# Kernel tuning notes

Measured on AMD Instinct MI355X. Metric: run time of the kernel, lower is better.

The kernel has to match this reference:

```python
import jax, jax.numpy as jnp
import numpy as np

N = 20000      # nodes
L = 64         # seq_length
E = 64         # emb_size
V = 30000      # vocab_size
HG = 128       # gnn_hidden_size
HT = 128       # text_hidden_size
NE = 640000    # edges
EPS = 1e-12


def _normalize(x):
    # F.normalize(x, p=2, dim=1) on [N, E, L]
    n = jnp.sqrt(jnp.sum(x * x, axis=1, keepdims=True))
    return x / jnp.maximum(n, EPS)


def gcn_conv(x, W, b, src_idx, dst_idx, n_nodes):
    # PyG GCNConv: add self-loops, symmetric normalization D^-1/2 (A+I) D^-1/2 (X W) + b
    h = x @ W                                            # [N, out]
    deg = jnp.zeros((n_nodes,), h.dtype).at[dst_idx].add(1.0) + 1.0  # incl. self-loop
    dinv = jax.lax.rsqrt(deg)
    norm = dinv[src_idx] * dinv[dst_idx]                 # [NE]
    msg = h[src_idx] * norm[:, None]                     # gather + scale
    out = jnp.zeros_like(h).at[dst_idx].add(msg)         # scatter-add to targets
    out = out + h * (dinv * dinv)[:, None]               # self-loop term
    return out + b


def setup_inputs() -> dict:
    key = jax.random.key(0)
    ks = jax.random.split(key, 12)
    rn = lambda k, shape: jax.random.normal(k, shape, jnp.float32) * 0.02
    return {
        "src": jax.random.randint(ks[0], (N, L), 0, V),
        "seg": jax.random.randint(ks[1], (N, L), 0, 3),
        "edge_index": jax.random.randint(ks[2], (2, NE), 0, N),
        "src_emb": rn(ks[3], (V, E)),
        "seg_emb": rn(ks[4], (3, E)),
        "w": jnp.ones((L,), jnp.float32),
        "Wq1": rn(ks[5], (E, HT)), "bq1": jnp.zeros((HT,), jnp.float32),
        "Wq2": rn(ks[6], (HT, E)), "bq2": jnp.zeros((E,), jnp.float32),
        "Wg1": rn(ks[7], (E, HG)), "bg1": jnp.zeros((HG,), jnp.float32),
        "Wg2": rn(ks[8], (HG, E)), "bg2": jnp.zeros((E,), jnp.float32),
        "Wl": rn(ks[9], (E, E)),   "bl": jnp.zeros((E,), jnp.float32),
    }


def reference(src, seg, edge_index, src_emb, seg_emb, w, Wq1, bq1, Wq2, bq2,
              Wg1, bg1, Wg2, bg2, Wl, bl):
    # --- LiteratureEmbedding ---
    se = src_emb[src]                 # [N, L, E]
    ge = seg_emb[seg]                 # [N, L, E]
    sv = se.reshape(-1, E, L)         # raw view (matches torch .view, not transpose)
    gv = ge.reshape(-1, E, L)
    f = (_normalize(w * sv) + _normalize(gv)).sum(-1)   # [N, E]
    # --- query MLP ---
    x = jax.nn.relu(f @ Wq1 + bq1) @ Wq2 + bq2
    # --- two GCN layers ---
    si, di = edge_index[0], edge_index[1]
    x = jax.nn.relu(gcn_conv(x, Wg1, bg1, si, di, N))
    x = jax.nn.relu(gcn_conv(x, Wg2, bg2, si, di, N))
    # --- output linear (dropout is identity in eval) ---
    return x @ Wl + bl
```

## Files before the change

kernel.cpp:

```cpp
#include <hip/hip_runtime.h>

#if defined(__has_builtin)
#if __has_builtin(__builtin_amdgcn_readlane)
#define READLANE(v, l) __builtin_amdgcn_readlane((v), (l))
#else
#define READLANE(v, l) __shfl((v), (l))
#endif
#else
#define READLANE(v, l) __shfl((v), (l))
#endif
__device__ __forceinline__ float readlane_f(float v, int l) {
    return __uint_as_float(READLANE(__float_as_uint(v), l));
}

__device__ __forceinline__ unsigned short f2bf(float x) {
    unsigned u = __float_as_uint(x);
    u += 0x7FFFu + ((u >> 16) & 1u);
    return (unsigned short)(u >> 16);
}
__device__ __forceinline__ float bfl(unsigned u) { return __uint_as_float(u << 16); }
__device__ __forceinline__ float bfh(unsigned u) { return __uint_as_float(u & 0xFFFF0000u); }

#define CAPLOG 8
#define EPB 10

__global__ __launch_bounds__(256) void hist_k(
    const int* __restrict__ di, int ne, int* __restrict__ bhist)
{
    __shared__ int lh[512];
    const int t = threadIdx.x;
    for (int i = t; i < 512; i += 256) lh[i] = 0;
    __syncthreads();
    const int base = blockIdx.x * (256 * EPB);
    #pragma unroll
    for (int r = 0; r < EPB; ++r) {
        int i = base + r * 256 + t;
        if (i < ne) atomicAdd(&lh[di[i] >> 6], 1);
    }
    __syncthreads();
    for (int i = t; i < 512; i += 256)
        if (lh[i]) atomicAdd(&bhist[i], lh[i]);
}

__global__ __launch_bounds__(256) void scan_k(
    const int* __restrict__ bhist, int* __restrict__ boff,
    int* __restrict__ bcur, int nb,
    unsigned* __restrict__ Cz, unsigned* __restrict__ Az)
{
    __shared__ int sh[512];
    const int t = threadIdx.x;
    for (int i = t; i < 512; i += 256) sh[i] = (i < nb) ? bhist[i] : 0;
    __syncthreads();
    if (t == 0) {
        int run = 0;
        for (int i = 0; i < nb; ++i) { int v = sh[i]; sh[i] = run; run += v; }
    }
    __syncthreads();
    for (int i = t; i < 512; i += 256)
        if (i < nb) { boff[i] = sh[i]; bcur[i] = sh[i]; }
    if (t < 32) { Cz[t] = 0u; Az[t] = 0u; }
}

__global__ __launch_bounds__(256) void prep0b_k(
    const int* __restrict__ si, const int* __restrict__ di, int ne,
    int* __restrict__ bcur, unsigned* __restrict__ pairs, int pB,
    const float* __restrict__ src_emb, unsigned short* __restrict__ sbf, int ve)
{
    const int t = threadIdx.x;
    if ((int)blockIdx.x < pB) {
        __shared__ int lh[512];
        __shared__ int lbase[512];
        for (int i = t; i < 512; i += 256) lh[i] = 0;
        __syncthreads();
        int bb[EPB], rk[EPB];
        unsigned pk[EPB];
        const int base = blockIdx.x * (256 * EPB);
        #pragma unroll
        for (int r = 0; r < EPB; ++r) {
            int i = base + r * 256 + t;
            if (i < ne) {
                int d = di[i], s = si[i];
                int b = d >> 6;
                bb[r] = b;
                rk[r] = atomicAdd(&lh[b], 1);
                pk[r] = ((unsigned)(d & 63) << 20) | (unsigned)s;
            } else bb[r] = -1;
        }
        __syncthreads();
        for (int i = t; i < 512; i += 256)
            if (lh[i]) lbase[i] = atomicAdd(&bcur[i], lh[i]);
        __syncthreads();
        #pragma unroll
        for (int r = 0; r < EPB; ++r)
            if (bb[r] >= 0) pairs[lbase[bb[r]] + rk[r]] = pk[r];
        return;
    }
    int i = (((int)blockIdx.x - pB) * 256 + t) * 4;
    if (i + 3 < ve) {
        float4 v = *(const float4*)&src_emb[i];
        ushort4 u;
        u.x = f2bf(v.x); u.y = f2bf(v.y); u.z = f2bf(v.z); u.w = f2bf(v.w);
        *(ushort4*)&sbf[i] = u;
    } else {
        for (; i < ve; ++i) sbf[i] = f2bf(src_emb[i]);
    }
}

__global__ __launch_bounds__(256) void binfill_k(
    const unsigned* __restrict__ pairs, const int* __restrict__ bhist,
    const int* __restrict__ boff, int* __restrict__ edge_off,
    int* __restrict__ deg, int nN)
{
    __shared__ int cntL[64];
    __shared__ int slotsL[64 * 256];
    const int t = threadIdx.x;
    const int b = blockIdx.x;
    if (t < 64) cntL[t] = 0;
    __syncthreads();
    const int ne_b = bhist[b];
    const int st   = boff[b];
    for (int k = t; k < ne_b; k += 256) {
        unsigned pk = pairs[st + k];
        int dl = (int)(pk >> 20);
        int s  = (int)(pk & 0xFFFFFu);
        int p  = atomicAdd(&cntL[dl], 1);
        if (p < 256) slotsL[dl * 256 + p] = s << 7;
    }
    __syncthreads();
    if (t < 64) {
        int node = (b << 6) + t;
        if (node < nN) deg[node] = cntL[t];
    }
    const int wv = t >> 6, j = t & 63;
    const int dl = wv * 16 + (j >> 2);
    const int k0 = j & 3;
    const int node = (b << 6) + dl;
    if (node < nN) {
        const int c = min(cntL[dl], 256);
        for (int k = k0; k < c; k += 4)
            edge_off[((long)node << CAPLOG) + k] = slotsL[dl * 256 + k];
    }
}

__global__ __launch_bounds__(256) void prep1_k(
    const int* __restrict__ src, const int* __restrict__ seg,
    const unsigned short* __restrict__ sbf, const float* __restrict__ seg_emb,
    const float* __restrict__ wvec, float* __restrict__ f, int nN)
{
    __shared__ float scr[4][16 * 66];
    const int t = threadIdx.x;
    const int wid = t >> 6, q = t & 63;
    const long n = (long)blockIdx.x * 4 + wid;
    if (n >= nN) return;
    const int grp = q >> 4, c = q & 15;

    const int off = src[n * 64 + q] << 7;
    const int sg  = seg[n * 64 + q];
    const float e0 = seg_emb[q], e1 = seg_emb[64 + q], e2 = seg_emb[128 + q];
    const char* base = (const char*)sbf;

    uint2 dreg[16];
    #pragma unroll
    for (int i = 0; i < 16; ++i) {
        int ro = __shfl(off, i * 4 + grp);
        dreg[i] = *(const uint2*)(base + (ro + c * 8));
    }

    float t0 = 0.f, t1 = 0.f, t2 = 0.f, t3 = 0.f;
    #pragma unroll
    for (int i = 0; i < 16; ++i) {
        float v0 = bfl(dreg[i].x);
        float v1 = bfh(dreg[i].x);
        float v2 = bfl(dreg[i].y);
        float v3 = bfh(dreg[i].y);
        t0 += v0 * v0; t1 += v1 * v1; t2 += v2 * v2; t3 += v3 * v3;
    }
    t0 += __shfl_xor(t0, 16); t0 += __shfl_xor(t0, 32);
    t1 += __shfl_xor(t1, 16); t1 += __shfl_xor(t1, 32);
    t2 += __shfl_xor(t2, 16); t2 += __shfl_xor(t2, 32);
    t3 += __shfl_xor(t3, 16); t3 += __shfl_xor(t3, 32);

    const float4 wv = *(const float4*)&wvec[c * 4];
    float4 cf;
    cf.x = wv.x / fmaxf(fabsf(wv.x) * sqrtf(t0), 1e-12f);
    cf.y = wv.y / fmaxf(fabsf(wv.y) * sqrtf(t1), 1e-12f);
    cf.z = wv.z / fmaxf(fabsf(wv.z) * sqrtf(t2), 1e-12f);
    cf.w = wv.w / fmaxf(fabsf(wv.w) * sqrtf(t3), 1e-12f);

    unsigned long long b0 = __ballot(sg == 0);
    unsigned long long b1 = __ballot(sg == 1);
    float n0 = (float)__popcll(b0), n1 = (float)__popcll(b1);
    float n2 = 64.f - n0 - n1;
    float g2 = n0 * e0 * e0 + n1 * e1 * e1 + n2 * e2 * e2;
    float rg = 1.f / fmaxf(sqrtf(g2), 1e-12f);
    float p0 = e0 * rg, p1 = e1 * rg, p2 = e2 * rg;
    #pragma unroll
    for (int m = 1; m < 64; m <<= 1) {
        p0 += __shfl_xor(p0, m);
        p1 += __shfl_xor(p1, m);
        p2 += __shfl_xor(p2, m);
    }

    float* sw = scr[wid];
    #pragma unroll
    for (int i = 0; i < 16; ++i) {
        float po = bfl(dreg[i].x) * cf.x + bfh(dreg[i].x) * cf.y
                 + bfl(dreg[i].y) * cf.z + bfh(dreg[i].y) * cf.w;
        sw[c * 66 + i * 4 + grp] = po;
    }
    float out = 0.f;
    #pragma unroll
    for (int c2 = 0; c2 < 16; ++c2)
        out += sw[c2 * 66 + q];

    const float dg = (sg == 0) ? p0 : ((sg == 1) ? p1 : p2);
    f[n * 64 + q] = out + dg;
}

#define ACC8(d, a, b)                                                    \
    { (a).x += bfl((d).x); (a).y += bfh((d).x);                          \
      (a).z += bfl((d).y); (a).w += bfh((d).y);                          \
      (b).x += bfl((d).z); (b).y += bfh((d).z);                          \
      (b).z += bfl((d).w); (b).w += bfh((d).w); }

__device__ __forceinline__ void csr_gather16(const char* __restrict__ hb,
                                             const int* __restrict__ eo,
                                             int dn, int j, int zoff,
                                             float4& s0, float4& s1)
{
    const int grp = j >> 3;
    const int col = (j & 7) << 4;
    float4 a0 = make_float4(0.f, 0.f, 0.f, 0.f), a1 = a0;
    float4 b0 = a0, b1 = a0;
    for (int e = 0; e < dn; e += 64) {
        const int cnt = min(dn - e, 64);
        const int eoff = (e + j < dn) ? eo[e + j] : zoff;
        int m = 0;
        for (; m + 16 <= cnt; m += 16) {
            int o0 = __shfl(eoff, m + grp);
            int o1 = __shfl(eoff, m + 8 + grp);
            uint4 d0 = *(const uint4*)(hb + (o0 + col));
            uint4 d1 = *(const uint4*)(hb + (o1 + col));
            ACC8(d0, a0, a1); ACC8(d1, b0, b1);
        }
        for (; m < cnt; m += 8) {
            int o = __shfl(eoff, m + grp);
            uint4 d = *(const uint4*)(hb + (o + col));
            ACC8(d, a0, a1);
        }
    }
    a0.x += b0.x; a0.y += b0.y; a0.z += b0.z; a0.w += b0.w;
    a1.x += b1.x; a1.y += b1.y; a1.z += b1.z; a1.w += b1.w;
    #pragma unroll
    for (int m = 8; m < 64; m <<= 1) {
        a0.x += __shfl_xor(a0.x, m); a0.y += __shfl_xor(a0.y, m);
        a0.z += __shfl_xor(a0.z, m); a0.w += __shfl_xor(a0.w, m);
        a1.x += __shfl_xor(a1.x, m); a1.y += __shfl_xor(a1.y, m);
        a1.z += __shfl_xor(a1.z, m); a1.w += __shfl_xor(a1.w, m);
    }
    s0 = a0; s1 = a1;
}

__device__ __forceinline__ void bf_row16(const char* hb, long rowoff, int col,
                                         float4& v0, float4& v1) {
    uint4 d = *(const uint4*)(hb + rowoff + col);
    v0.x = bfl(d.x); v0.y = bfh(d.x); v0.z = bfl(d.y); v0.w = bfh(d.y);
    v1.x = bfl(d.z); v1.y = bfh(d.z); v1.z = bfl(d.w); v1.w = bfh(d.w);
}

template <bool S2_BIAS>
__device__ __forceinline__ void dense_pair_body(
    float* Wh, float* F, float* H,
    const float* __restrict__ W1, const float* __restrict__ b1,
    const float* __restrict__ W2, const float* __restrict__ b2,
    const int* __restrict__ deg, unsigned short* __restrict__ out,
    int row0, int nrows, int t)
{
    for (int i = t * 4; i < 32 * 128; i += 1024)
        *(float4*)&Wh[i] = *(const float4*)&W1[i];
    __syncthreads();

    const int jg = t & 31, rslot = t >> 5;
    const int j0 = jg * 4;
    float4 acc0, acc1;
    {
        float4 b4 = *(const float4*)&b1[j0];
        acc0 = b4; acc1 = b4;
    }
    #pragma unroll 2
    for (int k = 0; k < 32; k += 4) {
        float4 w0 = *(float4*)&Wh[(k + 0) * 128 + j0];
        float4 w1 = *(float4*)&Wh[(k + 1) * 128 + j0];
        float4 w2 = *(float4*)&Wh[(k + 2) * 128 + j0];
        float4 w3 = *(float4*)&Wh[(k + 3) * 128 + j0];
        float4 fa = *(float4*)&F[rslot * 64 + k];
        float4 fb = *(float4*)&F[(rslot + 8) * 64 + k];
        acc0.x += fa.x * w0.x + fa.y * w1.x + fa.z * w2.x + fa.w * w3.x;
        acc0.y += fa.x * w0.y + fa.y * w1.y + fa.z * w2.y + fa.w * w3.y;
        acc0.z += fa.x * w0.z + fa.y * w1.z + fa.z * w2.z + fa.w * w3.z;
        acc0.w += fa.x * w0.w + fa.y * w1.w + fa.z * w2.w + fa.w * w3.w;
        acc1.x += fb.x * w0.x + fb.y * w1.x + fb.z * w2.x + fb.w * w3.x;
        acc1.y += fb.x * w0.y + fb.y * w1.y + fb.z * w2.y + fb.w * w3.y;
        acc1.z += fb.x * w0.z + fb.y * w1.z + fb.z * w2.z + fb.w * w3.z;
        acc1.w += fb.x * w0.w + fb.y * w1.w + fb.z * w2.w + fb.w * w3.w;
    }
    __syncthreads();
    for (int i = t * 4; i < 32 * 128; i += 1024)
        *(float4*)&Wh[i] = *(const float4*)&W1[32 * 128 + i];
    __syncthreads();
    #pragma unroll 2
    for (int k = 0; k < 32; k += 4) {
        float4 w0 = *(float4*)&Wh[(k + 0) * 128 + j0];
        float4 w1 = *(float4*)&Wh[(k + 1) * 128 + j0];
        float4 w2 = *(float4*)&Wh[(k + 2) * 128 + j0];
        float4 w3 = *(float4*)&Wh[(k + 3) * 128 + j0];
        float4 fa = *(float4*)&F[rslot * 64 + 32 + k];
        float4 fb = *(float4*)&F[(rslot + 8) * 64 + 32 + k];
        acc0.x += fa.x * w0.x + fa.y * w1.x + fa.z * w2.x + fa.w * w3.x;
        acc0.y += fa.x * w0.y + fa.y * w1.y + fa.z * w2.y + fa.w * w3.y;
        acc0.z += fa.x * w0.z + fa.y * w1.z + fa.z * w2.z + fa.w * w3.z;
        acc0.w += fa.x * w0.w + fa.y * w1.w + fa.z * w2.w + fa.w * w3.w;
        acc1.x += fb.x * w0.x + fb.y * w1.x + fb.z * w2.x + fb.w * w3.x;
        acc1.y += fb.x * w0.y + fb.y * w1.y + fb.z * w2.y + fb.w * w3.y;
        acc1.z += fb.x * w0.z + fb.y * w1.z + fb.z * w2.z + fb.w * w3.z;
        acc1.w += fb.x * w0.w + fb.y * w1.w + fb.z * w2.w + fb.w * w3.w;
    }
    {
        float4 v;
        v.x = fmaxf(acc0.x, 0.f); v.y = fmaxf(acc0.y, 0.f);
        v.z = fmaxf(acc0.z, 0.f); v.w = fmaxf(acc0.w, 0.f);
        *(float4*)&H[rslot * 128 + j0] = v;
        v.x = fmaxf(acc1.x, 0.f); v.y = fmaxf(acc1.y, 0.f);
        v.z = fmaxf(acc1.z, 0.f); v.w = fmaxf(acc1.w, 0.f);
        *(float4*)&H[(rslot + 8) * 128 + j0] = v;
    }
    __syncthreads();

    for (int i = t * 4; i < 64 * 64; i += 1024)
        *(float4*)&Wh[i] = *(const float4*)&W2[i];
    __syncthreads();
    const int jg2 = t & 15, r2 = t >> 4;
    const int j02 = jg2 * 4;
    float4 acc = S2_BIAS ? *(const float4*)&b2[j02]
                         : make_float4(0.f, 0.f, 0.f, 0.f);
    #pragma unroll 2
    for (int k = 0; k < 64; k += 4) {
        float4 w0 = *(float4*)&Wh[(k + 0) * 64 + j02];
        float4 w1 = *(float4*)&Wh[(k + 1) * 64 + j02];
        float4 w2 = *(float4*)&Wh[(k + 2) * 64 + j02];
        float4 w3 = *(float4*)&Wh[(k + 3) * 64 + j02];
        float4 fq = *(float4*)&H[r2 * 128 + k];
        acc.x += fq.x * w0.x + fq.y * w1.x + fq.z * w2.x + fq.w * w3.x;
        acc.y += fq.x * w0.y + fq.y * w1.y + fq.z * w2.y + fq.w * w3.y;
        acc.z += fq.x * w0.z + fq.y * w1.z + fq.z * w2.z + fq.w * w3.z;
        acc.w += fq.x * w0.w + fq.y * w1.w + fq.z * w2.w + fq.w * w3.w;
    }
    __syncthreads();
    for (int i = t * 4; i < 64 * 64; i += 1024)
        *(float4*)&Wh[i] = *(const float4*)&W2[64 * 64 + i];
    __syncthreads();
    #pragma unroll 2
    for (int k = 0; k < 64; k += 4) {
        float4 w0 = *(float4*)&Wh[(k + 0) * 64 + j02];
        float4 w1 = *(float4*)&Wh[(k + 1) * 64 + j02];
        float4 w2 = *(float4*)&Wh[(k + 2) * 64 + j02];
        float4 w3 = *(float4*)&Wh[(k + 3) * 64 + j02];
        float4 fq = *(float4*)&H[r2 * 128 + 64 + k];
        acc.x += fq.x * w0.x + fq.y * w1.x + fq.z * w2.x + fq.w * w3.x;
        acc.y += fq.x * w0.y + fq.y * w1.y + fq.z * w2.y + fq.w * w3.y;
        acc.z += fq.x * w0.z + fq.y * w1.z + fq.z * w2.z + fq.w * w3.z;
        acc.w += fq.x * w0.w + fq.y * w1.w + fq.z * w2.w + fq.w * w3.w;
    }
    const int r = row0 + r2;
    if (r < nrows) {
        float sc = rsqrtf((float)deg[r] + 1.0f);
        ushort4 v;
        v.x = f2bf(acc.x * sc); v.y = f2bf(acc.y * sc);
        v.z = f2bf(acc.z * sc); v.w = f2bf(acc.w * sc);
        *(ushort4*)&out[(long)r * 64 + j02] = v;
    }
}

template <bool S2_BIAS>
__global__ __launch_bounds__(256, 5) void fused2_k(
    const float* __restrict__ in, const float* __restrict__ W1,
    const float* __restrict__ b1, const float* __restrict__ W2,
    const float* __restrict__ b2, const int* __restrict__ deg,
    unsigned short* __restrict__ out, int nrows)
{
    __shared__ __align__(16) float Wh[32 * 128];
    __shared__ __align__(16) float F[16 * 64];
    __shared__ __align__(16) float H[16 * 128];
    const int t = threadIdx.x;
    const int row0 = blockIdx.x * 16;

    for (int i = t * 4; i < 16 * 64; i += 1024) {
        int r = i >> 6;
        float4 v = make_float4(0.f, 0.f, 0.f, 0.f);
        if (row0 + r < nrows) v = *(const float4*)&in[(long)row0 * 64 + i];
        *(float4*)&F[i] = v;
    }
    dense_pair_body<S2_BIAS>(Wh, F, H, W1, b1, W2, b2, deg, out, row0, nrows, t);
}

__global__ __launch_bounds__(256, 5) void gcnfused_k(
    const unsigned short* __restrict__ C, const int* __restrict__ deg,
    const int* __restrict__ edge_off,
    const float* __restrict__ W1, const float* __restrict__ b1,
    const float* __restrict__ W2, unsigned short* __restrict__ out,
    int nrows, int zoff)
{
    __shared__ __align__(16) float Wh[32 * 128];
    __shared__ __align__(16) float F[16 * 64];
    __shared__ __align__(16) float H[16 * 128];
    const int t = threadIdx.x;
    const int row0 = blockIdx.x * 16;
    const int wv = t >> 6, j = t & 63;
    const int col = (j & 7) << 4;

    const char* hb = (const char*)C;
    #pragma unroll
    for (int i = 0; i < 4; ++i) {
        const int r = wv * 4 + i;
        const int node = row0 + r;
        if (node < nrows) {
            float4 s0, s1, v0, v1;
            csr_gather16(hb, edge_off + ((long)node << CAPLOG),
                         deg[node], j, zoff, s0, s1);
            bf_row16(hb, (long)node << 7, col, v0, v1);
            float dv = rsqrtf((float)deg[node] + 1.0f);
            if ((j >> 3) == 0) {
                float4 ra, rb;
                ra.x = dv * (v0.x + s0.x); ra.y = dv * (v0.y + s0.y);
                ra.z = dv * (v0.z + s0.z); ra.w = dv * (v0.w + s0.w);
                rb.x = dv * (v1.x + s1.x); rb.y = dv * (v1.y + s1.y);
                rb.z = dv * (v1.z + s1.z); rb.w = dv * (v1.w + s1.w);
                *(float4*)&F[r * 64 + j * 8]     = ra;
                *(float4*)&F[r * 64 + j * 8 + 4] = rb;
            }
        } else if ((j >> 3) == 0) {
            *(float4*)&F[r * 64 + j * 8]     = make_float4(0.f, 0.f, 0.f, 0.f);
            *(float4*)&F[r * 64 + j * 8 + 4] = make_float4(0.f, 0.f, 0.f, 0.f);
        }
    }
    dense_pair_body<false>(Wh, F, H, W1, b1, W2, nullptr, deg, out, row0, nrows, t);
}

__global__ __launch_bounds__(256) void gatherout_k(
    const unsigned short* __restrict__ hp, const int* __restrict__ deg,
    const int* __restrict__ edge_off,
    const float* __restrict__ bg2, const float* __restrict__ Wl,
    const float* __restrict__ bl, float* __restrict__ out, int n, int zoff)
{
    __shared__ __align__(16) float WlL[64 * 64];
    __shared__ __align__(16) float vS[4][64];
    const int t = threadIdx.x;
    for (int i = t * 4; i < 64 * 64; i += 1024)
        *(float4*)&WlL[i] = *(const float4*)&Wl[i];
    __syncthreads();

    const int row0 = blockIdx.x * 16;
    const int wv = t >> 6, j = t & 63;
    const int col = (j & 7) << 4;
    const char* hb = (const char*)hp;
    const float blj = bl[j];
    const float4 bgA = *(const float4*)&bg2[(j & 7) * 8];
    const float4 bgB = *(const float4*)&bg2[(j & 7) * 8 + 4];

    #pragma unroll
    for (int i = 0; i < 4; ++i) {
        const int node = row0 + wv * 4 + i;
        if (node >= n) continue;
        float4 s0, s1, v0, v1;
        csr_gather16(hb, edge_off + ((long)node << CAPLOG),
                     deg[node], j, zoff, s0, s1);
        bf_row16(hb, (long)node << 7, col, v0, v1);
        const float dv = rsqrtf((float)deg[node] + 1.0f);
        float4 fa, fb;
        fa.x = fmaxf(dv * (v0.x + s0.x) + bgA.x, 0.f);
        fa.y = fmaxf(dv * (v0.y + s0.y) + bgA.y, 0.f);
        fa.z = fmaxf(dv * (v0.z + s0.z) + bgA.z, 0.f);
        fa.w = fmaxf(dv * (v0.w + s0.w) + bgA.w, 0.f);
        fb.x = fmaxf(dv * (v1.x + s1.x) + bgB.x, 0.f);
        fb.y = fmaxf(dv * (v1.y + s1.y) + bgB.y, 0.f);
        fb.z = fmaxf(dv * (v1.z + s1.z) + bgB.z, 0.f);
        fb.w = fmaxf(dv * (v1.w + s1.w) + bgB.w, 0.f);
        if ((j >> 3) == 0) {
            *(float4*)&vS[wv][j * 8]     = fa;
            *(float4*)&vS[wv][j * 8 + 4] = fb;
        }
        const float v = vS[wv][j];

        float o = blj;
        #pragma unroll 4
        for (int k = 0; k < 64; k += 4) {
            float vk0 = readlane_f(v, k + 0);
            float vk1 = readlane_f(v, k + 1);
            float vk2 = readlane_f(v, k + 2);
            float vk3 = readlane_f(v, k + 3);
            o += vk0 * WlL[(k + 0) * 64 + j] + vk1 * WlL[(k + 1) * 64 + j]
               + vk2 * WlL[(k + 2) * 64 + j] + vk3 * WlL[(k + 3) * 64 + j];
        }
        out[(long)node * 64 + j] = o;
    }
}

extern "C" void kernel_launch(void* const* d_in, const int* in_sizes, int n_in,
                              void* d_out, int out_size, void* d_ws, size_t ws_size,
                              hipStream_t stream) {
    const int*   src     = (const int*)  d_in[0];
    const int*   seg     = (const int*)  d_in[1];
    const int*   ei      = (const int*)  d_in[2];
    const float* src_emb = (const float*)d_in[3];
    const float* seg_emb = (const float*)d_in[4];
    const float* w       = (const float*)d_in[5];
    const float* Wq1     = (const float*)d_in[6];
    const float* bq1     = (const float*)d_in[7];
    const float* Wq2     = (const float*)d_in[8];
    const float* bq2     = (const float*)d_in[9];
    const float* Wg1     = (const float*)d_in[10];
    const float* bg1     = (const float*)d_in[11];
    const float* Wg2     = (const float*)d_in[12];
    const float* bg2     = (const float*)d_in[13];
    const float* Wl      = (const float*)d_in[14];
    const float* bl      = (const float*)d_in[15];
    float* out = (float*)d_out;

    const int N  = in_sizes[0] / 64;
    const int NE = in_sizes[2] / 2;
    const int VE = in_sizes[3];
    const int* si = ei;
    const int* di = ei + NE;
    const int NB = (N + 63) >> 6;

    const size_t NEpad = ((size_t)NE + 3) & ~(size_t)3;
    const size_t VEpad = ((size_t)VE + 7) & ~(size_t)7;
    int* bhist = (int*)d_ws;
    int* boff  = bhist + 512;
    int* bcur  = boff + 512;
    int* deg   = bcur + 512;
    int* edge_off = deg + (((size_t)N + 3) & ~(size_t)3);
    unsigned* pairs = (unsigned*)(edge_off + ((size_t)N << CAPLOG));
    unsigned short* sbf = (unsigned short*)(pairs + NEpad);
    float* A32 = (float*)(sbf + VEpad);
    unsigned short* Cbf = (unsigned short*)(A32 + (size_t)N * 64);
    unsigned short* Abf = Cbf + (size_t)N * 64 + 64;
    const int zoff = N << 7;

    dim3 b256(256);
    const int convB = (VE + 1023) / 1024;
    const int eBig  = (NE + 256 * EPB - 1) / (256 * EPB);
    const int nB    = (N + 3) / 4;
    const int fB    = (N + 15) / 16;

    hipMemsetAsync(bhist, 0, 512 * sizeof(int), stream);

    hist_k<<<eBig, b256, 0, stream>>>(di, NE, bhist);
    scan_k<<<1, b256, 0, stream>>>(bhist, boff, bcur, NB,
                                   (unsigned*)(Cbf + (size_t)N * 64),
                                   (unsigned*)(Abf + (size_t)N * 64));
    prep0b_k<<<eBig + convB, b256, 0, stream>>>(si, di, NE, bcur, pairs, eBig,
                                                src_emb, sbf, VE);
    binfill_k<<<NB, b256, 0, stream>>>(pairs, bhist, boff, edge_off, deg, N);

    prep1_k<<<nB, b256, 0, stream>>>(src, seg, sbf, seg_emb, w, A32, N);

    fused2_k<true><<<fB, b256, 0, stream>>>(A32, Wq1, bq1, Wq2, bq2,
                                            deg, Cbf, N);

    gcnfused_k<<<fB, b256, 0, stream>>>(Cbf, deg, edge_off,
                                        Wg1, bg1, Wg2, Abf, N, zoff);

    gatherout_k<<<fB, b256, 0, stream>>>(Abf, deg, edge_off, bg2,
                                         Wl, bl, out, N, zoff);
}
```

Before: 215.5 us.

## Merge preprocessing kernels and compute degree via global atomics in histogram pass

The bf16 conversion of the embedding table moves into the histogram kernel, and the per-node embedding/normalization work (formerly prep1_k) now runs as extra blocks of the edge-scatter kernel. This cuts one launch and lets independent work share a grid to fill the GPU. Node degree is now counted with global atomics on deg in the histogram pass instead of being written by binfill, so the memset grows to clear deg. The price is 640k extra global atomics and heavier shared-memory use in the merged scatter kernel.

```diff
diff --git a/kernel.cpp b/kernel.cpp
--- a/kernel.cpp
+++ b/kernel.cpp
@@ -24,22 +24,40 @@
 #define CAPLOG 8
 #define EPB 10
 
-__global__ __launch_bounds__(256) void hist_k(
-    const int* __restrict__ di, int ne, int* __restrict__ bhist)
-{
-    __shared__ int lh[512];
-    const int t = threadIdx.x;
-    for (int i = t; i < 512; i += 256) lh[i] = 0;
-    __syncthreads();
-    const int base = blockIdx.x * (256 * EPB);
-    #pragma unroll
-    for (int r = 0; r < EPB; ++r) {
-        int i = base + r * 256 + t;
-        if (i < ne) atomicAdd(&lh[di[i] >> 6], 1);
-    }
-    __syncthreads();
-    for (int i = t; i < 512; i += 256)
-        if (lh[i]) atomicAdd(&bhist[i], lh[i]);
+__global__ __launch_bounds__(256) void histconv_k(
+    const int* __restrict__ di, int ne, int* __restrict__ bhist,
+    int* __restrict__ deg, int eB,
+    const float* __restrict__ src_emb, unsigned short* __restrict__ sbf, int ve)
+{
+    const int t = threadIdx.x;
+    if ((int)blockIdx.x < eB) {
+        __shared__ int lh[512];
+        for (int i = t; i < 512; i += 256) lh[i] = 0;
+        __syncthreads();
+        const int base = blockIdx.x * (256 * EPB);
+        #pragma unroll
+        for (int r = 0; r < EPB; ++r) {
+            int i = base + r * 256 + t;
+            if (i < ne) {
+                int d = di[i];
+                atomicAdd(&lh[d >> 6], 1);
+                atomicAdd(&deg[d], 1);
+            }
+        }
+        __syncthreads();
+        for (int i = t; i < 512; i += 256)
+            if (lh[i]) atomicAdd(&bhist[i], lh[i]);
+        return;
+    }
+    int i = (((int)blockIdx.x - eB) * 256 + t) * 4;
+    if (i + 3 < ve) {
+        float4 v = *(const float4*)&src_emb[i];
+        ushort4 u;
+        u.x = f2bf(v.x); u.y = f2bf(v.y); u.z = f2bf(v.z); u.w = f2bf(v.w);
+        *(ushort4*)&sbf[i] = u;
+    } else {
+        for (; i < ve; ++i) sbf[i] = f2bf(src_emb[i]);
+    }
 }
 
 __global__ __launch_bounds__(256) void scan_k(
@@ -61,15 +79,18 @@
     if (t < 32) { Cz[t] = 0u; Az[t] = 0u; }
 }
 
-__global__ __launch_bounds__(256) void prep0b_k(
+__global__ __launch_bounds__(256) void scatemb_k(
     const int* __restrict__ si, const int* __restrict__ di, int ne,
     int* __restrict__ bcur, unsigned* __restrict__ pairs, int pB,
-    const float* __restrict__ src_emb, unsigned short* __restrict__ sbf, int ve)
-{
+    const int* __restrict__ src, const int* __restrict__ seg,
+    const unsigned short* __restrict__ sbf, const float* __restrict__ seg_emb,
+    const float* __restrict__ wvec, float* __restrict__ f, int nN)
+{
+    __shared__ __align__(16) float smem[4 * 16 * 66];
     const int t = threadIdx.x;
     if ((int)blockIdx.x < pB) {
-        __shared__ int lh[512];
-        __shared__ int lbase[512];
+        int* lh    = (int*)smem;
+        int* lbase = (int*)smem + 512;
         for (int i = t; i < 512; i += 256) lh[i] = 0;
         __syncthreads();
         int bb[EPB], rk[EPB];
@@ -95,21 +116,77 @@
             if (bb[r] >= 0) pairs[lbase[bb[r]] + rk[r]] = pk[r];
         return;
     }
-    int i = (((int)blockIdx.x - pB) * 256 + t) * 4;
-    if (i + 3 < ve) {
-        float4 v = *(const float4*)&src_emb[i];
-        ushort4 u;
-        u.x = f2bf(v.x); u.y = f2bf(v.y); u.z = f2bf(v.z); u.w = f2bf(v.w);
-        *(ushort4*)&sbf[i] = u;
-    } else {
-        for (; i < ve; ++i) sbf[i] = f2bf(src_emb[i]);
-    }
+    const int wid = t >> 6, q = t & 63;
+    const long n = ((long)blockIdx.x - pB) * 4 + wid;
+    if (n >= nN) return;
+    const int grp = q >> 4, c = q & 15;
+
+    const int off = src[n * 64 + q] << 7;
+    const int sg  = seg[n * 64 + q];
+    const float e0 = seg_emb[q], e1 = seg_emb[64 + q], e2 = seg_emb[128 + q];
+    const char* base = (const char*)sbf;
+
+    uint2 dreg[16];
+    #pragma unroll
+    for (int i = 0; i < 16; ++i) {
+        int ro = __shfl(off, i * 4 + grp);
+        dreg[i] = *(const uint2*)(base + (ro + c * 8));
+    }
+
+    float t0 = 0.f, t1 = 0.f, t2 = 0.f, t3 = 0.f;
+    #pragma unroll
+    for (int i = 0; i < 16; ++i) {
+        float v0 = bfl(dreg[i].x);
+        float v1 = bfh(dreg[i].x);
+        float v2 = bfl(dreg[i].y);
+        float v3 = bfh(dreg[i].y);
+        t0 += v0 * v0; t1 += v1 * v1; t2 += v2 * v2; t3 += v3 * v3;
+    }
+    t0 += __shfl_xor(t0, 16); t0 += __shfl_xor(t0, 32);
+    t1 += __shfl_xor(t1, 16); t1 += __shfl_xor(t1, 32);
+    t2 += __shfl_xor(t2, 16); t2 += __shfl_xor(t2, 32);
+    t3 += __shfl_xor(t3, 16); t3 += __shfl_xor(t3, 32);
+
+    const float4 wv = *(const float4*)&wvec[c * 4];
+    float4 cf;
+    cf.x = wv.x / fmaxf(fabsf(wv.x) * sqrtf(t0), 1e-12f);
+    cf.y = wv.y / fmaxf(fabsf(wv.y) * sqrtf(t1), 1e-12f);
+    cf.z = wv.z / fmaxf(fabsf(wv.z) * sqrtf(t2), 1e-12f);
+    cf.w = wv.w / fmaxf(fabsf(wv.w) * sqrtf(t3), 1e-12f);
+
+    unsigned long long b0 = __ballot(sg == 0);
+    unsigned long long b1 = __ballot(sg == 1);
+    float n0 = (float)__popcll(b0), n1 = (float)__popcll(b1);
+    float n2 = 64.f - n0 - n1;
+    float g2 = n0 * e0 * e0 + n1 * e1 * e1 + n2 * e2 * e2;
+    float rg = 1.f / fmaxf(sqrtf(g2), 1e-12f);
+    float p0 = e0 * rg, p1 = e1 * rg, p2 = e2 * rg;
+    #pragma unroll
+    for (int m = 1; m < 64; m <<= 1) {
+        p0 += __shfl_xor(p0, m);
+        p1 += __shfl_xor(p1, m);
+        p2 += __shfl_xor(p2, m);
+    }
+
+    float* sw = smem + wid * (16 * 66);
+    #pragma unroll
+    for (int i = 0; i < 16; ++i) {
+        float po = bfl(dreg[i].x) * cf.x + bfh(dreg[i].x) * cf.y
+                 + bfl(dreg[i].y) * cf.z + bfh(dreg[i].y) * cf.w;
+        sw[c * 66 + i * 4 + grp] = po;
+    }
+    float out = 0.f;
+    #pragma unroll
+    for (int c2 = 0; c2 < 16; ++c2)
+        out += sw[c2 * 66 + q];
+
+    const float dg = (sg == 0) ? p0 : ((sg == 1) ? p1 : p2);
+    f[n * 64 + q] = out + dg;
 }
 
 __global__ __launch_bounds__(256) void binfill_k(
     const unsigned* __restrict__ pairs, const int* __restrict__ bhist,
-    const int* __restrict__ boff, int* __restrict__ edge_off,
-    int* __restrict__ deg, int nN)
+    const int* __restrict__ boff, int* __restrict__ edge_off, int nN)
 {
     __shared__ int cntL[64];
     __shared__ int slotsL[64 * 256];
@@ -127,10 +204,6 @@
         if (p < 256) slotsL[dl * 256 + p] = s << 7;
     }
     __syncthreads();
-    if (t < 64) {
-        int node = (b << 6) + t;
-        if (node < nN) deg[node] = cntL[t];
-    }
     const int wv = t >> 6, j = t & 63;
     const int dl = wv * 16 + (j >> 2);
     const int k0 = j & 3;
@@ -140,81 +213,6 @@
         for (int k = k0; k < c; k += 4)
             edge_off[((long)node << CAPLOG) + k] = slotsL[dl * 256 + k];
     }
-}
-
-__global__ __launch_bounds__(256) void prep1_k(
-    const int* __restrict__ src, const int* __restrict__ seg,
-    const unsigned short* __restrict__ sbf, const float* __restrict__ seg_emb,
-    const float* __restrict__ wvec, float* __restrict__ f, int nN)
-{
-    __shared__ float scr[4][16 * 66];
-    const int t = threadIdx.x;
-    const int wid = t >> 6, q = t & 63;
-    const long n = (long)blockIdx.x * 4 + wid;
-    if (n >= nN) return;
-    const int grp = q >> 4, c = q & 15;
-
-    const int off = src[n * 64 + q] << 7;
-    const int sg  = seg[n * 64 + q];
-    const float e0 = seg_emb[q], e1 = seg_emb[64 + q], e2 = seg_emb[128 + q];
-    const char* base = (const char*)sbf;
-
-    uint2 dreg[16];
-    #pragma unroll
-    for (int i = 0; i < 16; ++i) {
-        int ro = __shfl(off, i * 4 + grp);
-        dreg[i] = *(const uint2*)(base + (ro + c * 8));
-    }
-
-    float t0 = 0.f, t1 = 0.f, t2 = 0.f, t3 = 0.f;
-    #pragma unroll
-    for (int i = 0; i < 16; ++i) {
-        float v0 = bfl(dreg[i].x);
-        float v1 = bfh(dreg[i].x);
-        float v2 = bfl(dreg[i].y);
-        float v3 = bfh(dreg[i].y);
-        t0 += v0 * v0; t1 += v1 * v1; t2 += v2 * v2; t3 += v3 * v3;
-    }
-    t0 += __shfl_xor(t0, 16); t0 += __shfl_xor(t0, 32);
-    t1 += __shfl_xor(t1, 16); t1 += __shfl_xor(t1, 32);
-    t2 += __shfl_xor(t2, 16); t2 += __shfl_xor(t2, 32);
-    t3 += __shfl_xor(t3, 16); t3 += __shfl_xor(t3, 32);
-
-    const float4 wv = *(const float4*)&wvec[c * 4];
-    float4 cf;
-    cf.x = wv.x / fmaxf(fabsf(wv.x) * sqrtf(t0), 1e-12f);
-    cf.y = wv.y / fmaxf(fabsf(wv.y) * sqrtf(t1), 1e-12f);
-    cf.z = wv.z / fmaxf(fabsf(wv.z) * sqrtf(t2), 1e-12f);
-    cf.w = wv.w / fmaxf(fabsf(wv.w) * sqrtf(t3), 1e-12f);
-
-    unsigned long long b0 = __ballot(sg == 0);
-    unsigned long long b1 = __ballot(sg == 1);
-    float n0 = (float)__popcll(b0), n1 = (float)__popcll(b1);
-    float n2 = 64.f - n0 - n1;
-    float g2 = n0 * e0 * e0 + n1 * e1 * e1 + n2 * e2 * e2;
-    float rg = 1.f / fmaxf(sqrtf(g2), 1e-12f);
-    float p0 = e0 * rg, p1 = e1 * rg, p2 = e2 * rg;
-    #pragma unroll
-    for (int m = 1; m < 64; m <<= 1) {
-        p0 += __shfl_xor(p0, m);
-        p1 += __shfl_xor(p1, m);
-        p2 += __shfl_xor(p2, m);
-    }
-
-    float* sw = scr[wid];
-    #pragma unroll
-    for (int i = 0; i < 16; ++i) {
-        float po = bfl(dreg[i].x) * cf.x + bfh(dreg[i].x) * cf.y
-                 + bfl(dreg[i].y) * cf.z + bfh(dreg[i].y) * cf.w;
-        sw[c * 66 + i * 4 + grp] = po;
-    }
-    float out = 0.f;
-    #pragma unroll
-    for (int c2 = 0; c2 < 16; ++c2)
-        out += sw[c2 * 66 + q];
-
-    const float dg = (sg == 0) ? p0 : ((sg == 1) ? p1 : p2);
-    f[n * 64 + q] = out + dg;
 }
 
 #define ACC8(d, a, b)                                                    \
@@ -533,13 +531,14 @@
     const int* di = ei + NE;
     const int NB = (N + 63) >> 6;
 
+    const size_t Npad  = ((size_t)N + 3) & ~(size_t)3;
     const size_t NEpad = ((size_t)NE + 3) & ~(size_t)3;
     const size_t VEpad = ((size_t)VE + 7) & ~(size_t)7;
     int* bhist = (int*)d_ws;
     int* boff  = bhist + 512;
     int* bcur  = boff + 512;
     int* deg   = bcur + 512;
-    int* edge_off = deg + (((size_t)N + 3) & ~(size_t)3);
+    int* edge_off = deg + Npad;
     unsigned* pairs = (unsigned*)(edge_off + ((size_t)N << CAPLOG));
     unsigned short* sbf = (unsigned short*)(pairs + NEpad);
     float* A32 = (float*)(sbf + VEpad);
@@ -553,17 +552,16 @@
     const int nB    = (N + 3) / 4;
     const int fB    = (N + 15) / 16;
 
-    hipMemsetAsync(bhist, 0, 512 * sizeof(int), stream);
-
-    hist_k<<<eBig, b256, 0, stream>>>(di, NE, bhist);
+    hipMemsetAsync(bhist, 0, (1536 + Npad) * sizeof(int), stream);
+
+    histconv_k<<<eBig + convB, b256, 0, stream>>>(di, NE, bhist, deg, eBig,
+                                                  src_emb, sbf, VE);
     scan_k<<<1, b256, 0, stream>>>(bhist, boff, bcur, NB,
                                    (unsigned*)(Cbf + (size_t)N * 64),
                                    (unsigned*)(Abf + (size_t)N * 64));
-    prep0b_k<<<eBig + convB, b256, 0, stream>>>(si, di, NE, bcur, pairs, eBig,
-                                                src_emb, sbf, VE);
-    binfill_k<<<NB, b256, 0, stream>>>(pairs, bhist, boff, edge_off, deg, N);
-
-    prep1_k<<<nB, b256, 0, stream>>>(src, seg, sbf, seg_emb, w, A32, N);
+    scatemb_k<<<eBig + nB, b256, 0, stream>>>(si, di, NE, bcur, pairs, eBig,
+                                              src, seg, sbf, seg_emb, w, A32, N);
+    binfill_k<<<NB, b256, 0, stream>>>(pairs, bhist, boff, edge_off, N);
 
     fused2_k<true><<<fB, b256, 0, stream>>>(A32, Wq1, bq1, Wq2, bq2,
                                             deg, Cbf, N);
```

Result: slower. 233.7 us (+8.5%).
